# Kernel optimization log

Measured on AMD Instinct MI355X. Metric: run time of the kernel, lower is better.

The kernel has to match this reference:

```python
import jax, jax.numpy as jnp
import numpy as np

N_HEAD = 16


def setup_inputs() -> dict:
    key = jax.random.key(0)
    ks = jax.random.split(key, 5)
    B, T, C = 2, 2048, 1024
    s = 1.0 / np.sqrt(C)
    inp = {
        "x": jax.random.normal(ks[0], (B, T, C), dtype=jnp.float32),
        "Wq": jax.random.normal(ks[1], (C, C), dtype=jnp.float32) * s,
        "bq": jnp.zeros((C,), dtype=jnp.float32),
        "Wk": jax.random.normal(ks[2], (C, C), dtype=jnp.float32) * s,
        "bk": jnp.zeros((C,), dtype=jnp.float32),
        "Wv": jax.random.normal(ks[3], (C, C), dtype=jnp.float32) * s,
        "bv": jnp.zeros((C,), dtype=jnp.float32),
        "Wp": jax.random.normal(ks[4], (C, C), dtype=jnp.float32) * s,
        "bp": jnp.zeros((C,), dtype=jnp.float32),
    }
    return inp


def reference(x, Wq, bq, Wk, bk, Wv, bv, Wp, bp):
    B, T, C = x.shape
    H = N_HEAD
    D = C // H
    # linear projections (torch Linear: x @ W.T + b)
    q = (x @ Wq.T + bq).reshape(B, T, H, D)
    k = (x @ Wk.T + bk).reshape(B, T, H, D)
    v = (x @ Wv.T + bv).reshape(B, T, H, D)
    # scaled dot-product attention (NO causal mask in original forward)
    att = jnp.einsum("bthd,bshd->bhts", q, k) * (1.0 / np.sqrt(D))
    att = jax.nn.softmax(att, axis=-1)
    y = jnp.einsum("bhts,bshd->bthd", att, v).reshape(B, T, C)
    # output projection (dropouts are identity at p=0 / eval)
    return y @ Wp.T + bp
```

## Files before the change

kernel.cpp:

```cpp
#include <hip/hip_runtime.h>
#include <hip/hip_bf16.h>

typedef __attribute__((ext_vector_type(4))) float f32x4;
typedef __attribute__((ext_vector_type(16))) float f32x16;
typedef __attribute__((ext_vector_type(8))) short bf16x8;
typedef __attribute__((ext_vector_type(2))) unsigned int u32x2;

#define T_SEQ 2048
#define C_DIM 1024
#define NH 16
#define DHD 64

__device__ __forceinline__ unsigned cvtpk_bf16(float lo, float hi) {
    unsigned r;
    asm("v_cvt_pk_bf16_f32 %0, %1, %2" : "=v"(r) : "v"(lo), "v"(hi));
    return r;
}

__device__ __forceinline__ float exp2_hw(float x) {
    float r;
    asm("v_exp_f32 %0, %1" : "=v"(r) : "v"(x));
    return r;
}

__device__ __forceinline__ void async_copy16(void* lds, const void* g) {
    __builtin_amdgcn_global_load_lds(
        (const __attribute__((address_space(1))) unsigned int*)(uintptr_t)g,
        (__attribute__((address_space(3))) unsigned int*)(unsigned int)(uintptr_t)lds,
        16, 0, 0);
}

__global__ __launch_bounds__(256) void cvt_all(const float* __restrict__ x,
                                               const float* __restrict__ Wq, const float* __restrict__ Wk,
                                               const float* __restrict__ Wv, const float* __restrict__ Wp,
                                               __hip_bfloat16* __restrict__ xb,
                                               __hip_bfloat16* __restrict__ wf,
                                               __hip_bfloat16* __restrict__ wpb) {
    int i = blockIdx.x * blockDim.x + threadIdx.x;
    const float* src; __hip_bfloat16* dst; int off;
    if (i < 1048576) { src = x; dst = xb; off = i; }
    else {
        int j = i - 1048576; int wi = j >> 18; off = j & 262143;
        switch (wi) {
            case 0:  src = Wq; dst = wf;           break;
            case 1:  src = Wk; dst = wf + 1048576; break;
            case 2:  src = Wv; dst = wf + 2097152; break;
            default: src = Wp; dst = wpb;          break;
        }
    }
    float4 v = *(const float4*)(src + (size_t)off * 4);
    union { __hip_bfloat16 h[4]; u32x2 u; } p;
    p.h[0] = __float2bfloat16(v.x); p.h[1] = __float2bfloat16(v.y);
    p.h[2] = __float2bfloat16(v.z); p.h[3] = __float2bfloat16(v.w);
    *(u32x2*)(dst + (size_t)off * 4) = p.u;
}

__global__ __launch_bounds__(512) void gemm_qkv(const __hip_bfloat16* __restrict__ A,
                                                const __hip_bfloat16* __restrict__ Bw,
                                                const float* __restrict__ biasq,
                                                const float* __restrict__ biask,
                                                const float* __restrict__ biasv,
                                                __hip_bfloat16* __restrict__ oq,
                                                __hip_bfloat16* __restrict__ okk,
                                                __hip_bfloat16* __restrict__ ovt) {
    __shared__ __align__(16) char lds[131072];

    const int xcd = (int)blockIdx.x & 7, loc = (int)blockIdx.x >> 3;
    const int mloc = loc / 6, nloc = loc - mloc * 6;
    const int m0 = ((xcd & 3) * 4 + mloc) * 256;
    const int n0 = ((xcd >> 2) * 6 + nloc) * 256;

    const int tid = threadIdx.x;
    const int w = tid >> 6, l = tid & 63;
    const int wr = w >> 2, wc = w & 3;
    const int lg = l >> 4, lr = l & 15;

    const int sr0 = tid >> 3;
    const int sc0 = (tid & 7) * 16;
    const int gc0 = sc0 ^ ((sr0 & 7) << 4);
    const size_t goff = (size_t)sr0 * 2048 + gc0;

    const char* Ag = (const char*)A + (size_t)m0 * 2048;
    const char* Bg = (const char*)Bw + (size_t)n0 * 2048;

    auto STAGE_A = [&](int buf, int half, int kt) {
        const char* g = Ag + (size_t)(half * 128) * 2048 + kt * 128 + goff;
        char* d = lds + (buf * 2 + half) * 16384 + w * 1024;
        async_copy16(d, g);
        async_copy16(d + 8192, g + (size_t)64 * 2048);
    };
    auto STAGE_B = [&](int buf, int half, int kt) {
        const char* g = Bg + (size_t)(half * 128) * 2048 + kt * 128 + goff;
        char* d = lds + 65536 + (buf * 2 + half) * 16384 + w * 1024;
        async_copy16(d, g);
        async_copy16(d + 8192, g + (size_t)64 * 2048);
    };

    const int sw = (lr & 7) << 4;
    auto LDA = [&](bf16x8* af, int buf, int mq) {
        const char* base = lds + (buf * 2 + wr) * 16384;
        #pragma unroll
        for (int m = 0; m < 4; m++) {
            const int r = (mq * 4 + m) * 16 + lr;
            #pragma unroll
            for (int kk = 0; kk < 2; kk++)
                af[m * 2 + kk] = *(const bf16x8*)(base + r * 128 + ((kk * 64 + lg * 16) ^ sw));
        }
    };
    auto LDB = [&](bf16x8* bfv, int buf, int nq) {
        const char* base = lds + 65536 + (buf * 2 + (wc >> 1)) * 16384;
        #pragma unroll
        for (int n = 0; n < 2; n++) {
            const int r = (wc & 1) * 64 + (nq * 2 + n) * 16 + lr;
            #pragma unroll
            for (int kk = 0; kk < 2; kk++)
                bfv[n * 2 + kk] = *(const bf16x8*)(base + r * 128 + ((kk * 64 + lg * 16) ^ sw));
        }
    };

    f32x4 acc[8][4] = {};
    auto MF = [&](const bf16x8* af, const bf16x8* bfv, int mq, int nq) {
        #pragma unroll
        for (int m = 0; m < 4; m++)
            #pragma unroll
            for (int n = 0; n < 2; n++)
                #pragma unroll
                for (int kk = 0; kk < 2; kk++)
                    acc[mq * 4 + m][nq * 2 + n] = __builtin_amdgcn_mfma_f32_16x16x32_bf16(
                        af[m * 2 + kk], bfv[n * 2 + kk], acc[mq * 4 + m][nq * 2 + n], 0, 0, 0);
    };

#define PH_OPEN()  __builtin_amdgcn_sched_barrier(0); \
                   __builtin_amdgcn_s_barrier(); \
                   asm volatile("s_waitcnt lgkmcnt(0)" ::: "memory"); \
                   __builtin_amdgcn_sched_barrier(0); \
                   __builtin_amdgcn_s_setprio(1);
#define PH_CLOSE() __builtin_amdgcn_s_setprio(0); \
                   __builtin_amdgcn_sched_barrier(0); \
                   __builtin_amdgcn_s_barrier();
#define PH_CLOSE_VM() __builtin_amdgcn_s_setprio(0); \
                   asm volatile("s_waitcnt vmcnt(6)" ::: "memory"); \
                   __builtin_amdgcn_sched_barrier(0); \
                   __builtin_amdgcn_s_barrier();

    bf16x8 af[8], bf0[4], bf1[4];

    STAGE_B(0, 0, 0); STAGE_B(0, 1, 0); STAGE_A(0, 0, 0); STAGE_A(0, 1, 0);
    STAGE_B(1, 0, 1); STAGE_B(1, 1, 1); STAGE_A(1, 0, 1);
    asm volatile("s_waitcnt vmcnt(6)" ::: "memory");
    __builtin_amdgcn_sched_barrier(0);
    __builtin_amdgcn_s_barrier();

    for (int it = 0; it < 8; ++it) {
        const int t1 = 2 * it + 1;
        const int c2 = (2 * it + 2 < 16) ? 2 * it + 2 : 14;
        const int c3 = (2 * it + 3 < 16) ? 2 * it + 3 : 15;
        const int b2 = c2 & 1, b3 = c3 & 1;

        LDA(af, 0, 0); LDB(bf0, 0, 0);
        STAGE_A(1, 1, t1);
        PH_OPEN(); MF(af, bf0, 0, 0); PH_CLOSE();
        LDB(bf1, 0, 1);
        PH_OPEN(); MF(af, bf1, 0, 1); PH_CLOSE();
        LDA(af, 0, 1);
        STAGE_B(b2, 0, c2);
        PH_OPEN(); MF(af, bf1, 1, 1); PH_CLOSE();
        STAGE_B(b2, 1, c2); STAGE_A(b2, 0, c2);
        PH_OPEN(); MF(af, bf0, 1, 0); PH_CLOSE_VM();

        LDA(af, 1, 0); LDB(bf0, 1, 0);
        STAGE_A(b2, 1, c2);
        PH_OPEN(); MF(af, bf0, 0, 0); PH_CLOSE();
        LDB(bf1, 1, 1);
        PH_OPEN(); MF(af, bf1, 0, 1); PH_CLOSE();
        LDA(af, 1, 1);
        STAGE_B(b3, 0, c3);
        PH_OPEN(); MF(af, bf1, 1, 1); PH_CLOSE();
        STAGE_B(b3, 1, c3); STAGE_A(b3, 0, c3);
        PH_OPEN(); MF(af, bf0, 1, 0); PH_CLOSE_VM();
    }
#undef PH_OPEN
#undef PH_CLOSE
#undef PH_CLOSE_VM

    const int proj = n0 >> 10;
    if (proj < 2) {
        const float* bias = (proj == 0) ? biasq : biask;
        const float bsc = (proj == 0) ? 0.125f * 1.4426950408889634f : 1.0f;
        __hip_bfloat16* dst = (proj == 0) ? oq : okk;
        #pragma unroll
        for (int m = 0; m < 8; m++)
            #pragma unroll
            for (int n = 0; n < 4; n++)
                #pragma unroll
                for (int rr = 0; rr < 4; rr++) {
                    int row = m0 + wr * 128 + m * 16 + lg * 4 + rr;
                    int col = n0 + wc * 64 + n * 16 + lr;
                    int colL = col & (C_DIM - 1);
                    float val = (acc[m][n][rr] + bias[colL]) * bsc;
                    int b = row >> 11, t = row & 2047, hh = colL >> 6, dd = colL & 63;
                    dst[(((size_t)(b * NH + hh)) * T_SEQ + t) * DHD + dd] = __float2bfloat16(val);
                }
    } else {
        #pragma unroll
        for (int m = 0; m < 8; m++) {
            const int rowb = m0 + wr * 128 + m * 16 + lg * 4;
            const int b = rowb >> 11, t0 = rowb & 2047;
            #pragma unroll
            for (int n = 0; n < 4; n++) {
                int col = n0 + wc * 64 + n * 16 + lr;
                int colL = col & (C_DIM - 1);
                int hh = colL >> 6, dd = colL & 63;
                float bv = biasv[colL];
                union { __hip_bfloat16 h[4]; u32x2 u; } p;
                #pragma unroll
                for (int rr = 0; rr < 4; rr++)
                    p.h[rr] = __float2bfloat16(acc[m][n][rr] + bv);
                *(u32x2*)&ovt[(((size_t)(b * NH + hh)) * DHD + dd) * T_SEQ + t0] = p.u;
            }
        }
    }
}

__global__ __launch_bounds__(256) void gemm_proj(const __hip_bfloat16* __restrict__ A,
                                                 const __hip_bfloat16* __restrict__ Bw,
                                                 const float* __restrict__ biasp,
                                                 float* __restrict__ outf) {
    __shared__ __align__(16) char As[128 * 128];
    __shared__ __align__(16) char Bs[128 * 128];

    const int nwg = gridDim.x;
    const int cpx = nwg >> 3;
    const int wg = ((int)blockIdx.x & 7) * cpx + ((int)blockIdx.x >> 3);
    const int m0 = (wg & 31) * 128;
    const int n0 = (wg >> 5) * 128;

    const int tid = threadIdx.x;
    const int w = tid >> 6, l = tid & 63;
    const int wr = w >> 1, wc = w & 1;
    const int lg = l >> 4, lr = l & 15;

    const char* Ag = (const char*)A + (size_t)m0 * 2048;
    const char* Bg = (const char*)Bw + (size_t)n0 * 2048;
    const int lrow = l >> 3;
    const int scol = (l & 7) * 16;

    f32x4 acc[4][4] = {};

    for (int kt = 0; kt < 16; ++kt) {
        __syncthreads();
        #pragma unroll
        for (int i = 0; i < 4; i++) {
            const int rb = w * 32 + i * 8;
            const size_t go = (size_t)(rb + lrow) * 2048 + (size_t)kt * 128 + scol;
            async_copy16(&As[rb * 128], Ag + go);
            async_copy16(&Bs[rb * 128], Bg + go);
        }
        __syncthreads();
        #pragma unroll
        for (int kk = 0; kk < 2; kk++) {
            bf16x8 af[4], bfr[4];
            #pragma unroll
            for (int m = 0; m < 4; m++)
                af[m] = *(const bf16x8*)(&As[(wr * 64 + m * 16 + lr) * 128 + kk * 64 + lg * 16]);
            #pragma unroll
            for (int n = 0; n < 4; n++)
                bfr[n] = *(const bf16x8*)(&Bs[(wc * 64 + n * 16 + lr) * 128 + kk * 64 + lg * 16]);
            #pragma unroll
            for (int m = 0; m < 4; m++)
                #pragma unroll
                for (int n = 0; n < 4; n++)
                    acc[m][n] = __builtin_amdgcn_mfma_f32_16x16x32_bf16(af[m], bfr[n], acc[m][n], 0, 0, 0);
        }
    }

    #pragma unroll
    for (int m = 0; m < 4; m++)
        #pragma unroll
        for (int n = 0; n < 4; n++)
            #pragma unroll
            for (int r = 0; r < 4; r++) {
                int row = m0 + wr * 64 + m * 16 + lg * 4 + r;
                int col = n0 + wc * 64 + n * 16 + lr;
                outf[(size_t)row * C_DIM + col] = acc[m][n][r] + biasp[col];
            }
}

__global__ __launch_bounds__(256) void attn8(const __hip_bfloat16* __restrict__ Q,
                                             const __hip_bfloat16* __restrict__ K,
                                             const __hip_bfloat16* __restrict__ Vt,
                                             __hip_bfloat16* __restrict__ Y) {
    const int bid = blockIdx.x;
    const int xcd = bid & 7, slot = bid >> 3;
    const int head = xcd * 4 + (slot & 3);
    const int qblk = slot >> 2;

    const int tid = threadIdx.x;
    const int w = tid >> 6, l = tid & 63;
    const int lq = l & 31, hi = l >> 5;
    const int q0 = qblk * 128 + w * 32;

    __shared__ __align__(16) char Ks[3][8192];
    __shared__ __align__(16) char Vs[3][8192];
    __shared__ float bc[4][32];

    const char* Kb = (const char*)(K + (size_t)head * T_SEQ * DHD);
    const char* Vb = (const char*)(Vt + (size_t)head * DHD * T_SEQ);

    bf16x8 qf[4];
    {
        const char* qrow = (const char*)(Q + ((size_t)head * T_SEQ + q0 + lq) * DHD);
        #pragma unroll
        for (int t = 0; t < 4; t++) qf[t] = *(const bf16x8*)(qrow + t * 32 + hi * 16);
    }

    f32x16 yacc[2] = {};
    float ls0 = 0.f, ls1 = 0.f, ls2 = 0.f, ls3 = 0.f;

    const int o0 = (2 * w) * 1024 + l * 16;
    const int o1 = o0 + 1024;
    const int r0 = o0 >> 7, c0b = o0 & 127;
    const int r1 = o1 >> 7, c1b = o1 & 127;
    const int wads0 = r0 * 128 + (c0b ^ ((r0 & 7) << 4));
    const int wads1 = r1 * 128 + (c1b ^ ((r1 & 7) << 4));
    const char* vsrc0 = Vb + (size_t)r0 * (T_SEQ * 2) + c0b;
    const char* vsrc1 = Vb + (size_t)r1 * (T_SEQ * 2) + c1b;

    float4 kreg0, kreg1, vreg0, vreg1;
    auto stage_load = [&](int tile) {
        const char* kb2 = Kb + (size_t)tile * 8192;
        kreg0 = *(const float4*)(kb2 + o0);
        kreg1 = *(const float4*)(kb2 + o1);
        vreg0 = *(const float4*)(vsrc0 + (size_t)tile * 128);
        vreg1 = *(const float4*)(vsrc1 + (size_t)tile * 128);
    };
    auto stage_write = [&](int buf) {
        *(float4*)(&Ks[buf][wads0]) = kreg0;
        *(float4*)(&Ks[buf][wads1]) = kreg1;
        *(float4*)(&Vs[buf][wads0]) = vreg0;
        *(float4*)(&Vs[buf][wads1]) = vreg1;
    };

    auto qk = [&](int buf, f32x16& s0h, f32x16& s1h) {
        s0h = f32x16{}; s1h = f32x16{};
        const char* base0 = Ks[buf] + lq * 128;
        const char* base1 = Ks[buf] + (32 + lq) * 128;
        const int sw0 = (lq & 7) << 4;
        __builtin_amdgcn_s_setprio(1);
        #pragma unroll
        for (int t = 0; t < 4; t++) {
            bf16x8 kf0 = *(const bf16x8*)(base0 + ((t * 32 + hi * 16) ^ sw0));
            s0h = __builtin_amdgcn_mfma_f32_32x32x16_bf16(kf0, qf[t], s0h, 0, 0, 0);
        }
        #pragma unroll
        for (int t = 0; t < 4; t++) {
            bf16x8 kf1 = *(const bf16x8*)(base1 + ((t * 32 + hi * 16) ^ sw0));
            s1h = __builtin_amdgcn_mfma_f32_32x32x16_bf16(kf1, qf[t], s1h, 0, 0, 0);
        }
        __builtin_amdgcn_s_setprio(0);
    };

    auto sm_exp = [&](f32x16& a, f32x16& b) {
        #pragma unroll
        for (int r = 0; r < 16; r += 4) {
            a[r + 0] = exp2_hw(a[r + 0]); a[r + 1] = exp2_hw(a[r + 1]);
            a[r + 2] = exp2_hw(a[r + 2]); a[r + 3] = exp2_hw(a[r + 3]);
            b[r + 0] = exp2_hw(b[r + 0]); b[r + 1] = exp2_hw(b[r + 1]);
            b[r + 2] = exp2_hw(b[r + 2]); b[r + 3] = exp2_hw(b[r + 3]);
            ls0 += a[r + 0] + b[r + 0];
            ls1 += a[r + 1] + b[r + 1];
            ls2 += a[r + 2] + b[r + 2];
            ls3 += a[r + 3] + b[r + 3];
        }
    };

    auto pv = [&](int buf, const f32x16& a, const f32x16& b) {
        unsigned pw0[8], pw1[8];
        #pragma unroll
        for (int M = 0; M < 4; M++) {
            const int u = M * 4;
            pw0[M] = cvtpk_bf16(a[u + 0], a[u + 1]);
            pw1[M] = cvtpk_bf16(a[u + 2], a[u + 3]);
            pw0[M + 4] = cvtpk_bf16(b[u + 0], b[u + 1]);
            pw1[M + 4] = cvtpk_bf16(b[u + 2], b[u + 3]);
        }
        __builtin_amdgcn_s_setprio(1);
        #pragma unroll
        for (int t = 0; t < 4; t++) {
            u32x2 s0p = __builtin_amdgcn_permlane32_swap(pw0[2 * t], pw0[2 * t + 1], false, false);
            u32x2 s1p = __builtin_amdgcn_permlane32_swap(pw1[2 * t], pw1[2 * t + 1], false, false);
            union { unsigned u[4]; bf16x8 v; } af;
            af.u[0] = s0p.x; af.u[1] = s1p.x; af.u[2] = s0p.y; af.u[3] = s1p.y;
            #pragma unroll
            for (int dh = 0; dh < 2; dh++) {
                const int row = dh * 32 + lq;
                bf16x8 vf = *(const bf16x8*)(&Vs[buf][row * 128 + ((t * 32 + hi * 16) ^ ((row & 7) << 4))]);
                yacc[dh] = __builtin_amdgcn_mfma_f32_32x32x16_bf16(af.v, vf, yacc[dh], 0, 0, 0);
            }
        }
        __builtin_amdgcn_s_setprio(0);
    };

    f32x16 sA0, sA1, sB0, sB1;
    stage_load(0); stage_write(0);
    stage_load(1); stage_write(1);
    stage_load(2);
    __syncthreads();
    qk(0, sA0, sA1);

    for (int t = 0; t < 32; t += 2) {
        qk((t + 1) % 3, sB0, sB1);
        if (t + 2 < 32) {
            asm volatile("s_waitcnt vmcnt(0)" ::: "memory");
            stage_write((t + 2) % 3);
            if (t + 3 < 32) stage_load(t + 3);
        }
        sm_exp(sA0, sA1);
        pv(t % 3, sA0, sA1);
        asm volatile("s_waitcnt lgkmcnt(0)" ::: "memory");
        __builtin_amdgcn_s_barrier();
        __builtin_amdgcn_sched_barrier(0);

        const int t1 = t + 1;
        if (t1 + 1 < 32) qk((t1 + 1) % 3, sA0, sA1);
        if (t1 + 2 < 32) {
            asm volatile("s_waitcnt vmcnt(0)" ::: "memory");
            stage_write((t1 + 2) % 3);
            if (t1 + 3 < 32) stage_load(t1 + 3);
        }
        sm_exp(sB0, sB1);
        pv(t1 % 3, sB0, sB1);
        asm volatile("s_waitcnt lgkmcnt(0)" ::: "memory");
        __builtin_amdgcn_s_barrier();
        __builtin_amdgcn_sched_barrier(0);
    }

    float lsum = (ls0 + ls1) + (ls2 + ls3);
    lsum += __shfl_xor(lsum, 32);
    float inv = 1.0f / lsum;
    if (hi == 0) bc[w][lq] = inv;
    asm volatile("s_waitcnt lgkmcnt(0)" ::: "memory");
    __builtin_amdgcn_sched_barrier(0);

    const int b = head >> 4, h16 = head & 15;
    const size_t rowbase = (size_t)b * T_SEQ + q0;
    #pragma unroll
    for (int r = 0; r < 16; r++) {
        const int crow = (r & 3) + 8 * (r >> 2) + 4 * hi;
        const float iv = bc[w][crow];
        const size_t row = rowbase + crow;
        Y[row * C_DIM + h16 * DHD + lq]      = __float2bfloat16(yacc[0][r] * iv);
        Y[row * C_DIM + h16 * DHD + 32 + lq] = __float2bfloat16(yacc[1][r] * iv);
    }
}

extern "C" void kernel_launch(void* const* d_in, const int* in_sizes, int n_in,
                              void* d_out, int out_size, void* d_ws, size_t ws_size,
                              hipStream_t stream) {
    (void)in_sizes; (void)n_in; (void)out_size; (void)ws_size;
    const float* x  = (const float*)d_in[0];
    const float* Wq = (const float*)d_in[1];
    const float* bq = (const float*)d_in[2];
    const float* Wk = (const float*)d_in[3];
    const float* bk = (const float*)d_in[4];
    const float* Wv = (const float*)d_in[5];
    const float* bv = (const float*)d_in[6];
    const float* Wp = (const float*)d_in[7];
    const float* bp = (const float*)d_in[8];
    float* out = (float*)d_out;

    char* ws = (char*)d_ws;
    const size_t MC = (size_t)4096 * C_DIM;
    const size_t CC = (size_t)C_DIM * C_DIM;
    __hip_bfloat16* xb  = (__hip_bfloat16*)ws;  ws += MC * 2;
    __hip_bfloat16* wf  = (__hip_bfloat16*)ws;  ws += 3 * CC * 2;
    __hip_bfloat16* wpb = (__hip_bfloat16*)ws;  ws += CC * 2;
    __hip_bfloat16* qb  = (__hip_bfloat16*)ws;  ws += MC * 2;
    __hip_bfloat16* kb  = (__hip_bfloat16*)ws;  ws += MC * 2;
    __hip_bfloat16* vtb = (__hip_bfloat16*)ws;  ws += MC * 2;
    __hip_bfloat16* yb  = (__hip_bfloat16*)ws;  ws += MC * 2;

    cvt_all<<<8192, 256, 0, stream>>>(x, Wq, Wk, Wv, Wp, xb, wf, wpb);

    gemm_qkv<<<192, 512, 0, stream>>>(xb, wf, bq, bk, bv, qb, kb, vtb);

    attn8<<<512, 256, 0, stream>>>(qb, kb, vtb, yb);

    gemm_proj<<<256, 256, 0, stream>>>(yb, wpb, bp, out);
}
```

Measured before the change: 120.2 us.

## Split attention over two key halves and merge partials in a combine kernel

The attention kernel now splits the key/value sequence into two halves, launching twice as many blocks. Each block writes a normalized partial output and its softmax denominator to workspace. A new combine kernel blends the two partials, weighted by their denominators, into the head-interleaved layout. The aim is more parallelism and better occupancy across CUs. The cost is an extra launch, extra partial-output traffic, doubled per-block prologue work, and a correctness dependence on both halves sharing the same max reference in the exponent.

```diff
diff --git a/kernel.cpp b/kernel.cpp
--- a/kernel.cpp
+++ b/kernel.cpp
@@ -286,14 +286,18 @@
             }
 }
 
-__global__ __launch_bounds__(256) void attn8(const __hip_bfloat16* __restrict__ Q,
-                                             const __hip_bfloat16* __restrict__ K,
-                                             const __hip_bfloat16* __restrict__ Vt,
-                                             __hip_bfloat16* __restrict__ Y) {
+__global__ __launch_bounds__(256) void attn_part(const __hip_bfloat16* __restrict__ Q,
+                                                 const __hip_bfloat16* __restrict__ K,
+                                                 const __hip_bfloat16* __restrict__ Vt,
+                                                 __hip_bfloat16* __restrict__ pY,
+                                                 float* __restrict__ pL) {
     const int bid = blockIdx.x;
     const int xcd = bid & 7, slot = bid >> 3;
     const int head = xcd * 4 + (slot & 3);
-    const int qblk = slot >> 2;
+    const int rest = slot >> 2;
+    const int qblk = rest >> 1;
+    const int split = rest & 1;
+    const int tb = split * 16;
 
     const int tid = threadIdx.x;
     const int w = tid >> 6, l = tid & 63;
@@ -402,18 +406,18 @@
     };
 
     f32x16 sA0, sA1, sB0, sB1;
-    stage_load(0); stage_write(0);
-    stage_load(1); stage_write(1);
-    stage_load(2);
+    stage_load(tb); stage_write(0);
+    stage_load(tb + 1); stage_write(1);
+    stage_load(tb + 2);
     __syncthreads();
     qk(0, sA0, sA1);
 
-    for (int t = 0; t < 32; t += 2) {
+    for (int t = 0; t < 16; t += 2) {
         qk((t + 1) % 3, sB0, sB1);
-        if (t + 2 < 32) {
+        if (t + 2 < 16) {
             asm volatile("s_waitcnt vmcnt(0)" ::: "memory");
             stage_write((t + 2) % 3);
-            if (t + 3 < 32) stage_load(t + 3);
+            if (t + 3 < 16) stage_load(tb + t + 3);
         }
         sm_exp(sA0, sA1);
         pv(t % 3, sA0, sA1);
@@ -422,11 +426,11 @@
         __builtin_amdgcn_sched_barrier(0);
 
         const int t1 = t + 1;
-        if (t1 + 1 < 32) qk((t1 + 1) % 3, sA0, sA1);
-        if (t1 + 2 < 32) {
+        if (t1 + 1 < 16) qk((t1 + 1) % 3, sA0, sA1);
+        if (t1 + 2 < 16) {
             asm volatile("s_waitcnt vmcnt(0)" ::: "memory");
             stage_write((t1 + 2) % 3);
-            if (t1 + 3 < 32) stage_load(t1 + 3);
+            if (t1 + 3 < 16) stage_load(tb + t1 + 3);
         }
         sm_exp(sB0, sB1);
         pv(t1 % 3, sB0, sB1);
@@ -442,16 +446,41 @@
     asm volatile("s_waitcnt lgkmcnt(0)" ::: "memory");
     __builtin_amdgcn_sched_barrier(0);
 
-    const int b = head >> 4, h16 = head & 15;
-    const size_t rowbase = (size_t)b * T_SEQ + q0;
+    const size_t pbase = (size_t)(split * 32 + head) * T_SEQ + q0;
+    if (hi == 0) pL[pbase + lq] = lsum;
     #pragma unroll
     for (int r = 0; r < 16; r++) {
         const int crow = (r & 3) + 8 * (r >> 2) + 4 * hi;
         const float iv = bc[w][crow];
-        const size_t row = rowbase + crow;
-        Y[row * C_DIM + h16 * DHD + lq]      = __float2bfloat16(yacc[0][r] * iv);
-        Y[row * C_DIM + h16 * DHD + 32 + lq] = __float2bfloat16(yacc[1][r] * iv);
-    }
+        const size_t row = pbase + crow;
+        pY[row * 64 + lq]      = __float2bfloat16(yacc[0][r] * iv);
+        pY[row * 64 + 32 + lq] = __float2bfloat16(yacc[1][r] * iv);
+    }
+}
+
+__global__ __launch_bounds__(256) void attn_combine(const __hip_bfloat16* __restrict__ pY,
+                                                    const float* __restrict__ pL,
+                                                    __hip_bfloat16* __restrict__ yb) {
+    const int i = blockIdx.x * 256 + threadIdx.x;
+    const int dg = i & 7;
+    const int hrow = i >> 3;
+    const int trow = hrow & 2047;
+    const int head = hrow >> 11;
+    const size_t p0 = (size_t)head * T_SEQ + trow;
+    const float l0 = pL[p0], l1 = pL[32 * T_SEQ + p0];
+    const float rs = 1.0f / (l0 + l1);
+    const float w0 = l0 * rs, w1 = l1 * rs;
+    const bf16x8 y0 = *(const bf16x8*)(pY + p0 * 64 + dg * 8);
+    const bf16x8 y1 = *(const bf16x8*)(pY + (size_t)32 * T_SEQ * 64 + p0 * 64 + dg * 8);
+    union { __hip_bfloat16 h[8]; bf16x8 v; } o;
+    #pragma unroll
+    for (int j = 0; j < 8; j++) {
+        union { short s; __hip_bfloat16 h; } a, b;
+        a.s = y0[j]; b.s = y1[j];
+        o.h[j] = __float2bfloat16(__bfloat162float(a.h) * w0 + __bfloat162float(b.h) * w1);
+    }
+    const int b16 = head >> 4, h16 = head & 15;
+    *(bf16x8*)(yb + ((size_t)(b16 * T_SEQ + trow)) * C_DIM + h16 * DHD + dg * 8) = o.v;
 }
 
 extern "C" void kernel_launch(void* const* d_in, const int* in_sizes, int n_in,
@@ -479,12 +508,15 @@
     __hip_bfloat16* kb  = (__hip_bfloat16*)ws;  ws += MC * 2;
     __hip_bfloat16* vtb = (__hip_bfloat16*)ws;  ws += MC * 2;
     __hip_bfloat16* yb  = (__hip_bfloat16*)ws;  ws += MC * 2;
+    __hip_bfloat16* pY  = (__hip_bfloat16*)ws;  ws += (size_t)2 * 32 * T_SEQ * 64 * 2;
+    float*          pL  = (float*)ws;           ws += (size_t)2 * 32 * T_SEQ * 4;
 
     cvt_all<<<8192, 256, 0, stream>>>(x, Wq, Wk, Wv, Wp, xb, wf, wpb);
 
     gemm_qkv<<<192, 512, 0, stream>>>(xb, wf, bq, bk, bv, qb, kb, vtb);
 
-    attn8<<<512, 256, 0, stream>>>(qb, kb, vtb, yb);
+    attn_part<<<1024, 256, 0, stream>>>(qb, kb, vtb, pY, pL);
+    attn_combine<<<2048, 256, 0, stream>>>(pY, pL, yb);
 
     gemm_proj<<<256, 256, 0, stream>>>(yb, wpb, bp, out);
 }
```

New measurement: 125.9 us. 4.8% more time.

## Retile QKV GEMM to 128x384 tiles across 256 workgroups

Applied to the files above, without the earlier changes.

Changes the fused QKV projection GEMM from 256x256 tiles on 192 workgroups to 128x384 tiles on 256 workgroups, which fills all compute units on the device. The LDS staging, fragment loads, MFMA phase schedule and vmcnt waits are restructured to match the new tile shape. Because a tile can now span the Q/K/V boundary, the epilogue picks the projection per column fragment. The trade-off is lower arithmetic intensity per tile and more global traffic, in exchange for better occupancy and less tail imbalance.

```diff
diff --git a/kernel.cpp b/kernel.cpp
--- a/kernel.cpp
+++ b/kernel.cpp
@@ -65,10 +65,9 @@
                                                 __hip_bfloat16* __restrict__ ovt) {
     __shared__ __align__(16) char lds[131072];
 
-    const int xcd = (int)blockIdx.x & 7, loc = (int)blockIdx.x >> 3;
-    const int mloc = loc / 6, nloc = loc - mloc * 6;
-    const int m0 = ((xcd & 3) * 4 + mloc) * 256;
-    const int n0 = ((xcd >> 2) * 6 + nloc) * 256;
+    const int wg = ((int)blockIdx.x & 7) * 32 + ((int)blockIdx.x >> 3);
+    const int m0 = (wg & 31) * 128;
+    const int n0 = (wg >> 5) * 384;
 
     const int tid = threadIdx.x;
     const int w = tid >> 6, l = tid & 63;
@@ -84,50 +83,51 @@
     const char* Bg = (const char*)Bw + (size_t)n0 * 2048;
 
     auto STAGE_A = [&](int buf, int half, int kt) {
-        const char* g = Ag + (size_t)(half * 128) * 2048 + kt * 128 + goff;
-        char* d = lds + (buf * 2 + half) * 16384 + w * 1024;
+        const char* g = Ag + (size_t)(half * 64) * 2048 + kt * 128 + goff;
+        char* d = lds + (buf * 2 + half) * 8192 + w * 1024;
         async_copy16(d, g);
-        async_copy16(d + 8192, g + (size_t)64 * 2048);
     };
     auto STAGE_B = [&](int buf, int half, int kt) {
-        const char* g = Bg + (size_t)(half * 128) * 2048 + kt * 128 + goff;
-        char* d = lds + 65536 + (buf * 2 + half) * 16384 + w * 1024;
-        async_copy16(d, g);
-        async_copy16(d + 8192, g + (size_t)64 * 2048);
+        #pragma unroll
+        for (int p = 0; p < 3; p++) {
+            const char* g = Bg + (size_t)(half * 192 + p * 64) * 2048 + kt * 128 + goff;
+            char* d = lds + 32768 + (buf * 2 + half) * 24576 + p * 8192 + w * 1024;
+            async_copy16(d, g);
+        }
     };
 
     const int sw = (lr & 7) << 4;
-    auto LDA = [&](bf16x8* af, int buf, int mq) {
-        const char* base = lds + (buf * 2 + wr) * 16384;
+    auto LDA = [&](bf16x8* af, int buf) {
+        const char* base = lds + (buf * 2 + wr) * 8192;
         #pragma unroll
         for (int m = 0; m < 4; m++) {
-            const int r = (mq * 4 + m) * 16 + lr;
+            const int r = m * 16 + lr;
             #pragma unroll
             for (int kk = 0; kk < 2; kk++)
                 af[m * 2 + kk] = *(const bf16x8*)(base + r * 128 + ((kk * 64 + lg * 16) ^ sw));
         }
     };
     auto LDB = [&](bf16x8* bfv, int buf, int nq) {
-        const char* base = lds + 65536 + (buf * 2 + (wc >> 1)) * 16384;
+        const char* base = lds + 32768 + (buf * 2 + (wc >> 1)) * 24576;
         #pragma unroll
         for (int n = 0; n < 2; n++) {
-            const int r = (wc & 1) * 64 + (nq * 2 + n) * 16 + lr;
+            const int r = (wc & 1) * 96 + (nq * 2 + n) * 16 + lr;
             #pragma unroll
             for (int kk = 0; kk < 2; kk++)
                 bfv[n * 2 + kk] = *(const bf16x8*)(base + r * 128 + ((kk * 64 + lg * 16) ^ sw));
         }
     };
 
-    f32x4 acc[8][4] = {};
-    auto MF = [&](const bf16x8* af, const bf16x8* bfv, int mq, int nq) {
+    f32x4 acc[4][6] = {};
+    auto MF = [&](const bf16x8* af, const bf16x8* bfv, int nq) {
         #pragma unroll
         for (int m = 0; m < 4; m++)
             #pragma unroll
             for (int n = 0; n < 2; n++)
                 #pragma unroll
                 for (int kk = 0; kk < 2; kk++)
-                    acc[mq * 4 + m][nq * 2 + n] = __builtin_amdgcn_mfma_f32_16x16x32_bf16(
-                        af[m * 2 + kk], bfv[n * 2 + kk], acc[mq * 4 + m][nq * 2 + n], 0, 0, 0);
+                    acc[m][nq * 2 + n] = __builtin_amdgcn_mfma_f32_16x16x32_bf16(
+                        af[m * 2 + kk], bfv[n * 2 + kk], acc[m][nq * 2 + n], 0, 0, 0);
     };
 
 #define PH_OPEN()  __builtin_amdgcn_sched_barrier(0); \
@@ -138,16 +138,20 @@
 #define PH_CLOSE() __builtin_amdgcn_s_setprio(0); \
                    __builtin_amdgcn_sched_barrier(0); \
                    __builtin_amdgcn_s_barrier();
-#define PH_CLOSE_VM() __builtin_amdgcn_s_setprio(0); \
-                   asm volatile("s_waitcnt vmcnt(6)" ::: "memory"); \
+#define PH_CLOSE_VM2() __builtin_amdgcn_s_setprio(0); \
+                   asm volatile("s_waitcnt vmcnt(2)" ::: "memory"); \
                    __builtin_amdgcn_sched_barrier(0); \
                    __builtin_amdgcn_s_barrier();
-
-    bf16x8 af[8], bf0[4], bf1[4];
+#define PH_CLOSE_VM5() __builtin_amdgcn_s_setprio(0); \
+                   asm volatile("s_waitcnt vmcnt(5)" ::: "memory"); \
+                   __builtin_amdgcn_sched_barrier(0); \
+                   __builtin_amdgcn_s_barrier();
+
+    bf16x8 af[8], bfA[4], bfB[4], bfC[4];
 
     STAGE_B(0, 0, 0); STAGE_B(0, 1, 0); STAGE_A(0, 0, 0); STAGE_A(0, 1, 0);
-    STAGE_B(1, 0, 1); STAGE_B(1, 1, 1); STAGE_A(1, 0, 1);
-    asm volatile("s_waitcnt vmcnt(6)" ::: "memory");
+    STAGE_A(1, 0, 1); STAGE_A(1, 1, 1); STAGE_B(1, 0, 1);
+    asm volatile("s_waitcnt vmcnt(5)" ::: "memory");
     __builtin_amdgcn_sched_barrier(0);
     __builtin_amdgcn_s_barrier();
 
@@ -157,66 +161,57 @@
         const int c3 = (2 * it + 3 < 16) ? 2 * it + 3 : 15;
         const int b2 = c2 & 1, b3 = c3 & 1;
 
-        LDA(af, 0, 0); LDB(bf0, 0, 0);
-        STAGE_A(1, 1, t1);
-        PH_OPEN(); MF(af, bf0, 0, 0); PH_CLOSE();
-        LDB(bf1, 0, 1);
-        PH_OPEN(); MF(af, bf1, 0, 1); PH_CLOSE();
-        LDA(af, 0, 1);
+        LDA(af, 0); LDB(bfA, 0, 0);
+        STAGE_B(1, 1, t1);
+        PH_OPEN(); MF(af, bfA, 0); PH_CLOSE();
+        LDB(bfB, 0, 1);
+        STAGE_A(b2, 0, c2); STAGE_A(b2, 1, c2);
+        PH_OPEN(); MF(af, bfB, 1); PH_CLOSE();
+        LDB(bfC, 0, 2);
+        PH_OPEN(); MF(af, bfC, 2); PH_CLOSE_VM2();
+
+        LDA(af, 1); LDB(bfA, 1, 0);
         STAGE_B(b2, 0, c2);
-        PH_OPEN(); MF(af, bf1, 1, 1); PH_CLOSE();
-        STAGE_B(b2, 1, c2); STAGE_A(b2, 0, c2);
-        PH_OPEN(); MF(af, bf0, 1, 0); PH_CLOSE_VM();
-
-        LDA(af, 1, 0); LDB(bf0, 1, 0);
-        STAGE_A(b2, 1, c2);
-        PH_OPEN(); MF(af, bf0, 0, 0); PH_CLOSE();
-        LDB(bf1, 1, 1);
-        PH_OPEN(); MF(af, bf1, 0, 1); PH_CLOSE();
-        LDA(af, 1, 1);
+        PH_OPEN(); MF(af, bfA, 0); PH_CLOSE();
+        LDB(bfB, 1, 1);
+        STAGE_B(b2, 1, c2); STAGE_A(b3, 0, c3); STAGE_A(b3, 1, c3);
+        PH_OPEN(); MF(af, bfB, 1); PH_CLOSE();
+        LDB(bfC, 1, 2);
         STAGE_B(b3, 0, c3);
-        PH_OPEN(); MF(af, bf1, 1, 1); PH_CLOSE();
-        STAGE_B(b3, 1, c3); STAGE_A(b3, 0, c3);
-        PH_OPEN(); MF(af, bf0, 1, 0); PH_CLOSE_VM();
+        PH_OPEN(); MF(af, bfC, 2); PH_CLOSE_VM5();
     }
 #undef PH_OPEN
 #undef PH_CLOSE
-#undef PH_CLOSE_VM
-
-    const int proj = n0 >> 10;
-    if (proj < 2) {
-        const float* bias = (proj == 0) ? biasq : biask;
-        const float bsc = (proj == 0) ? 0.125f * 1.4426950408889634f : 1.0f;
-        __hip_bfloat16* dst = (proj == 0) ? oq : okk;
-        #pragma unroll
-        for (int m = 0; m < 8; m++)
-            #pragma unroll
-            for (int n = 0; n < 4; n++)
+#undef PH_CLOSE_VM2
+#undef PH_CLOSE_VM5
+
+    #pragma unroll
+    for (int m = 0; m < 4; m++) {
+        const int rowb = m0 + wr * 64 + m * 16 + lg * 4;
+        const int b = rowb >> 11, t0r = rowb & 2047;
+        #pragma unroll
+        for (int nf = 0; nf < 6; nf++) {
+            const int col = n0 + wc * 96 + nf * 16 + lr;
+            const int proj = col >> 10;
+            const int colL = col & 1023;
+            const int hh = colL >> 6, dd = colL & 63;
+            if (proj < 2) {
+                const float* bias = (proj == 0) ? biasq : biask;
+                const float bsc = (proj == 0) ? 0.125f * 1.4426950408889634f : 1.0f;
+                __hip_bfloat16* dst = (proj == 0) ? oq : okk;
                 #pragma unroll
                 for (int rr = 0; rr < 4; rr++) {
-                    int row = m0 + wr * 128 + m * 16 + lg * 4 + rr;
-                    int col = n0 + wc * 64 + n * 16 + lr;
-                    int colL = col & (C_DIM - 1);
-                    float val = (acc[m][n][rr] + bias[colL]) * bsc;
-                    int b = row >> 11, t = row & 2047, hh = colL >> 6, dd = colL & 63;
-                    dst[(((size_t)(b * NH + hh)) * T_SEQ + t) * DHD + dd] = __float2bfloat16(val);
+                    const int row = rowb + rr;
+                    float val = (acc[m][nf][rr] + bias[colL]) * bsc;
+                    dst[(((size_t)(b * NH + hh)) * T_SEQ + (row & 2047)) * DHD + dd] = __float2bfloat16(val);
                 }
-    } else {
-        #pragma unroll
-        for (int m = 0; m < 8; m++) {
-            const int rowb = m0 + wr * 128 + m * 16 + lg * 4;
-            const int b = rowb >> 11, t0 = rowb & 2047;
-            #pragma unroll
-            for (int n = 0; n < 4; n++) {
-                int col = n0 + wc * 64 + n * 16 + lr;
-                int colL = col & (C_DIM - 1);
-                int hh = colL >> 6, dd = colL & 63;
-                float bv = biasv[colL];
+            } else {
+                const float bv = biasv[colL];
                 union { __hip_bfloat16 h[4]; u32x2 u; } p;
                 #pragma unroll
                 for (int rr = 0; rr < 4; rr++)
-                    p.h[rr] = __float2bfloat16(acc[m][n][rr] + bv);
-                *(u32x2*)&ovt[(((size_t)(b * NH + hh)) * DHD + dd) * T_SEQ + t0] = p.u;
+                    p.h[rr] = __float2bfloat16(acc[m][nf][rr] + bv);
+                *(u32x2*)&ovt[(((size_t)(b * NH + hh)) * DHD + dd) * T_SEQ + t0r] = p.u;
             }
         }
     }
@@ -482,7 +477,7 @@
 
     cvt_all<<<8192, 256, 0, stream>>>(x, Wq, Wk, Wv, Wp, xb, wf, wpb);
 
-    gemm_qkv<<<192, 512, 0, stream>>>(xb, wf, bq, bk, bv, qb, kb, vtb);
+    gemm_qkv<<<256, 512, 0, stream>>>(xb, wf, bq, bk, bv, qb, kb, vtb);
 
     attn8<<<512, 256, 0, stream>>>(qb, kb, vtb, yb);
 
```

Result: no change. 119.2 us (-0.8%).
